# Performance work log

Hardware: AMD Instinct MI355X
Metric: run time of the kernel (lower is better)

Reference implementation:

```python
import jax, jax.numpy as jnp
import numpy as np

HIDDEN = 1024
HEADS = 16
HEAD_DIM = HIDDEN // HEADS
SCALE = HEAD_DIM ** -0.5


def setup_inputs() -> dict:
    key = jax.random.key(0)
    kx, kw, ko = jax.random.split(key, 3)
    x = jax.random.normal(kx, (2, 2048, HIDDEN), dtype=jnp.float32)
    # nn.Linear(hidden, 3*hidden, bias=False): weight shape [3*hidden, hidden]
    w_qkv = jax.random.normal(kw, (3 * HIDDEN, HIDDEN), dtype=jnp.float32) * (HIDDEN ** -0.5)
    w_out = jax.random.normal(ko, (HIDDEN, HIDDEN), dtype=jnp.float32) * (HIDDEN ** -0.5)
    return {"x": x, "w_qkv": w_qkv, "w_out": w_out}


def reference(x, w_qkv, w_out):
    b, s, d = x.shape
    qkv = jnp.einsum('bsd,ed->bse', x, w_qkv)  # [b,s,3d]
    q, k, v = jnp.split(qkv, 3, axis=-1)
    def heads(t):
        return t.reshape(b, s, HEADS, HEAD_DIM).transpose(0, 2, 1, 3)  # [b,h,s,hd]
    q, k, v = heads(q), heads(k), heads(v)
    scores = jnp.einsum('bhqd,bhkd->bhqk', q, k) * SCALE
    attn = jax.nn.softmax(scores, axis=-1)
    out = jnp.einsum('bhqk,bhkd->bhqd', attn, v)
    out = out.transpose(0, 2, 1, 3).reshape(b, s, d)
    return jnp.einsum('bsd,ed->bse', out, w_out)
```

## Files before the change

### kernel.cpp

```cpp
#include <hip/hip_runtime.h>
#include <hip/hip_bf16.h>
#include <stdint.h>

typedef __bf16 bf16;
typedef __bf16 bf16x8 __attribute__((ext_vector_type(8)));
typedef float f32x4 __attribute__((ext_vector_type(4)));
typedef float f32x16 __attribute__((ext_vector_type(16)));

#define HIDDEN 1024
#define HEADS  16
#define HD     64
#define SEQ    2048
#define BATCH  2
#define NTOK   (BATCH*SEQ)
#define E3     (3*HIDDEN)

static __device__ __forceinline__ uint32_t pkbf(float a, float b) {
  union { bf16 h[2]; uint32_t u; } x;
  x.h[0] = (bf16)a; x.h[1] = (bf16)b;
  return x.u;
}

__global__ __launch_bounds__(256) void k_convert(
    const float* __restrict__ x, const float* __restrict__ wqkv, const float* __restrict__ wout,
    bf16* __restrict__ xb, bf16* __restrict__ wqkvb, bf16* __restrict__ woutb)
{
  const int NX = NTOK*HIDDEN/4, NW = E3*HIDDEN/4;
  int i = blockIdx.x*256 + threadIdx.x;
  const float4* s; bf16* d; int o;
  if (i < NX)            { s=(const float4*)x;    d=xb;    o=i; }
  else if (i < NX+NW)    { s=(const float4*)wqkv; d=wqkvb; o=i-NX; }
  else                   { s=(const float4*)wout; d=woutb; o=i-NX-NW; }
  float4 v = s[o];
  union { bf16 b[4]; uint2 u; } p;
  p.b[0]=(bf16)v.x; p.b[1]=(bf16)v.y; p.b[2]=(bf16)v.z; p.b[3]=(bf16)v.w;
  *(uint2*)(d + (size_t)o*4) = p.u;
}

template<int EPI>
__global__ __launch_bounds__(256) void k_gemm(
    const bf16* __restrict__ A, const bf16* __restrict__ B,
    bf16* __restrict__ Oq, bf16* __restrict__ Ok, bf16* __restrict__ Ov,
    float* __restrict__ Of, int M, int N, int K, int nbn)
{
  __shared__ bf16 As[128*32];
  __shared__ bf16 Bs[128*32];
  const int t = threadIdx.x;
  const int lane = t & 63;
  const int w = t >> 6;
  const int g = lane >> 4;
  const int l15 = lane & 15;
  const int wm = (w >> 1) * 64, wn = (w & 1) * 64;
  const int bm = blockIdx.x / nbn, bn = blockIdx.x % nbn;
  const int brow = bm*128, bcol = bn*128;

  f32x4 acc[4][4];
  #pragma unroll
  for (int mi=0;mi<4;mi++)
    #pragma unroll
    for (int ni=0;ni<4;ni++)
      #pragma unroll
      for (int r=0;r<4;r++) acc[mi][ni][r] = 0.f;

  const int nk = K >> 5;
  for (int kt = 0; kt < nk; ++kt) {
    {
      int ch = w*128 + lane;
      const bf16* ga = A + (size_t)(brow + (ch>>2))*K + kt*32 + (ch&3)*8;
      __builtin_amdgcn_global_load_lds((const uint32_t*)ga, (uint32_t*)(As + (w*128)*8), 16, 0, 0);
      const bf16* gb = B + (size_t)(bcol + (ch>>2))*K + kt*32 + (ch&3)*8;
      __builtin_amdgcn_global_load_lds((const uint32_t*)gb, (uint32_t*)(Bs + (w*128)*8), 16, 0, 0);
      ch += 64;
      ga = A + (size_t)(brow + (ch>>2))*K + kt*32 + (ch&3)*8;
      __builtin_amdgcn_global_load_lds((const uint32_t*)ga, (uint32_t*)(As + (w*128+64)*8), 16, 0, 0);
      gb = B + (size_t)(bcol + (ch>>2))*K + kt*32 + (ch&3)*8;
      __builtin_amdgcn_global_load_lds((const uint32_t*)gb, (uint32_t*)(Bs + (w*128+64)*8), 16, 0, 0);
    }
    __syncthreads();
    bf16x8 af[4], bfr[4];
    #pragma unroll
    for (int mi=0;mi<4;mi++) af[mi]  = *(const bf16x8*)(As + (wm + mi*16 + l15)*32 + g*8);
    #pragma unroll
    for (int ni=0;ni<4;ni++) bfr[ni] = *(const bf16x8*)(Bs + (wn + ni*16 + l15)*32 + g*8);
    #pragma unroll
    for (int mi=0;mi<4;mi++)
      #pragma unroll
      for (int ni=0;ni<4;ni++)
        acc[mi][ni] = __builtin_amdgcn_mfma_f32_16x16x32_bf16(af[mi], bfr[ni], acc[mi][ni], 0, 0, 0);
    __syncthreads();
  }

  #pragma unroll
  for (int mi=0;mi<4;mi++) {
    #pragma unroll
    for (int ni=0;ni<4;ni++) {
      #pragma unroll
      for (int r=0;r<4;r++) {
        float val = acc[mi][ni][r];
        int m = brow + wm + mi*16 + 4*g + r;
        int e = bcol + wn + ni*16 + l15;
        if (EPI == 0) {
          int part = e >> 10, we = e & 1023;
          int hh = we >> 6, dd = we & 63;
          int b = m >> 11, sb = m & 2047;
          size_t idx = (((size_t)b*HEADS + hh)*SEQ + sb)*HD + dd;
          if (part == 0)      Oq[idx] = (bf16)(val * 0.125f);
          else if (part == 1) Ok[idx] = (bf16)val;
          else                Ov[idx] = (bf16)val;
        } else {
          Of[(size_t)m*HIDDEN + e] = val;
        }
      }
    }
  }
}

__global__ __launch_bounds__(256) void k_attn(
    const bf16* __restrict__ Qg, const bf16* __restrict__ Kg, const bf16* __restrict__ Vg,
    bf16* __restrict__ Og)
{
  __shared__ bf16 Kl[64*64];
  __shared__ bf16 Vt[64*64];
  const int t = threadIdx.x;
  const int lane = t & 63;
  const int w = t >> 6;
  const int h = lane >> 5;
  const int q = lane & 31;
  const int bh = blockIdx.x >> 4;
  const int qb = blockIdx.x & 15;
  const int q0 = qb*128 + w*32;
  const size_t bhS = (size_t)bh * SEQ * HD;

  bf16x8 qf[4];
  const bf16* qrow = Qg + bhS + (size_t)(q0 + q)*HD;
  #pragma unroll
  for (int s=0;s<4;s++) qf[s] = *(const bf16x8*)(qrow + 16*s + 8*h);

  f32x16 ot[2];
  #pragma unroll
  for (int mf=0;mf<2;mf++)
    #pragma unroll
    for (int r=0;r<16;r++) ot[mf][r]=0.f;
  float mrun = -3.0e38f, lrun = 0.f;

  for (int it=0; it<SEQ/64; ++it) {
    __syncthreads();
    {
      int ch = w*128 + lane;
      int row = ch>>3, o16 = ch&7;
      const bf16* gp = Kg + bhS + (size_t)(it*64+row)*HD + ((o16*8) ^ ((row&7)*8));
      __builtin_amdgcn_global_load_lds((const uint32_t*)gp, (uint32_t*)(Kl + (w*128)*8), 16, 0, 0);
      ch += 64; row = ch>>3; o16 = ch&7;
      gp = Kg + bhS + (size_t)(it*64+row)*HD + ((o16*8) ^ ((row&7)*8));
      __builtin_amdgcn_global_load_lds((const uint32_t*)gp, (uint32_t*)(Kl + (w*128+64)*8), 16, 0, 0);
    }
    {
      int kv0 = (t & 31)*2, d0 = (t>>5)*8;
      const bf16* vg = Vg + bhS + (size_t)(it*64 + kv0)*HD + d0;
      uint4 va = *(const uint4*)vg;
      uint4 vb = *(const uint4*)(vg + HD);
      const uint32_t* pa = (const uint32_t*)&va;
      const uint32_t* pb = (const uint32_t*)&vb;
      #pragma unroll
      for (int jj=0;jj<8;jj++) {
        int dd = d0 + jj;
        uint32_t lo = (jj&1) ? (pa[jj>>1] >> 16) : (pa[jj>>1] & 0xffffu);
        uint32_t hi = (jj&1) ? (pb[jj>>1] >> 16) : (pb[jj>>1] & 0xffffu);
        int byte = (dd*128 + kv0*2) ^ ((dd&7)<<4);
        *(uint32_t*)((char*)Vt + byte) = lo | (hi<<16);
      }
    }
    __syncthreads();

    f32x16 sf[2];
    #pragma unroll
    for (int mf=0;mf<2;mf++)
      #pragma unroll
      for (int r=0;r<16;r++) sf[mf][r]=0.f;
    #pragma unroll
    for (int s=0;s<4;s++) {
      #pragma unroll
      for (int mf=0;mf<2;mf++) {
        int row = mf*32 + q;
        int byte = (row*128 + 32*s + 16*h) ^ ((row&7)<<4);
        bf16x8 kf = *(const bf16x8*)((const char*)Kl + byte);
        sf[mf] = __builtin_amdgcn_mfma_f32_32x32x16_bf16(kf, qf[s], sf[mf], 0,0,0);
      }
    }

    float pm = -3.0e38f;
    #pragma unroll
    for (int mf=0;mf<2;mf++)
      #pragma unroll
      for (int r=0;r<16;r++) pm = fmaxf(pm, sf[mf][r]);
    pm = fmaxf(pm, __shfl_xor(pm, 32, 64));
    float mnew = fmaxf(mrun, pm);
    float alpha = __expf(mrun - mnew);
    float rs = 0.f;
    #pragma unroll
    for (int mf=0;mf<2;mf++)
      #pragma unroll
      for (int r=0;r<16;r++) { float p = __expf(sf[mf][r]-mnew); sf[mf][r]=p; rs += p; }
    rs += __shfl_xor(rs, 32, 64);
    lrun = lrun*alpha + rs;
    mrun = mnew;
    #pragma unroll
    for (int mf=0;mf<2;mf++)
      #pragma unroll
      for (int r=0;r<16;r++) ot[mf][r] *= alpha;

    #pragma unroll
    for (int s=0;s<4;s++) {
      const int f = s>>1, bb = 8*(s&1);
      uint32_t g0A = pkbf(sf[f][bb+0], sf[f][bb+1]);
      uint32_t g0B = pkbf(sf[f][bb+2], sf[f][bb+3]);
      uint32_t g1A = pkbf(sf[f][bb+4], sf[f][bb+5]);
      uint32_t g1B = pkbf(sf[f][bb+6], sf[f][bb+7]);
      uint32_t ownA = h ? g1A : g0A, ownB = h ? g1B : g0B;
      uint32_t sndA = h ? g0A : g1A, sndB = h ? g0B : g1B;
      uint32_t rcvA = __shfl_xor(sndA, 32, 64);
      uint32_t rcvB = __shfl_xor(sndB, 32, 64);
      union { uint32_t u[4]; bf16x8 v; } pf;
      if (h == 0) { pf.u[0]=ownA; pf.u[1]=ownB; pf.u[2]=rcvA; pf.u[3]=rcvB; }
      else        { pf.u[0]=rcvA; pf.u[1]=rcvB; pf.u[2]=ownA; pf.u[3]=ownB; }
      #pragma unroll
      for (int mf=0;mf<2;mf++) {
        int row = mf*32 + q;
        int byte = (row*128 + 32*s + 16*h) ^ ((row&7)<<4);
        bf16x8 vf = *(const bf16x8*)((const char*)Vt + byte);
        ot[mf] = __builtin_amdgcn_mfma_f32_32x32x16_bf16(vf, pf.v, ot[mf], 0,0,0);
      }
    }
  }

  float inv = 1.0f / lrun;
  int b = bh >> 4, head = bh & 15;
  size_t orow = ((size_t)b*SEQ + q0 + q)*HIDDEN + head*HD;
  #pragma unroll
  for (int mf=0;mf<2;mf++)
    #pragma unroll
    for (int r=0;r<16;r++) {
      int dd = mf*32 + (r&3) + 8*(r>>2) + 4*h;
      Og[orow + dd] = (bf16)(ot[mf][r]*inv);
    }
}

extern "C" void kernel_launch(void* const* d_in, const int* in_sizes, int n_in,
                              void* d_out, int out_size, void* d_ws, size_t ws_size,
                              hipStream_t stream)
{
  (void)in_sizes; (void)n_in; (void)out_size; (void)ws_size;
  const float* x    = (const float*)d_in[0];
  const float* wqkv = (const float*)d_in[1];
  const float* wout = (const float*)d_in[2];
  float* out = (float*)d_out;
  char* ws = (char*)d_ws;
  bf16* xb    = (bf16*)(ws);
  bf16* wqkvb = (bf16*)(ws + 8388608);
  bf16* woutb = (bf16*)(ws + 14680064);
  bf16* Q     = (bf16*)(ws + 16777216);
  bf16* K     = (bf16*)(ws + 25165824);
  bf16* V     = (bf16*)(ws + 33554432);
  bf16* O     = (bf16*)(ws + 41943040);

  k_convert<<<8192, 256, 0, stream>>>(x, wqkv, wout, xb, wqkvb, woutb);
  k_gemm<0><<<32*24, 256, 0, stream>>>(xb, wqkvb, Q, K, V, nullptr, NTOK, E3, HIDDEN, 24);
  k_attn<<<512, 256, 0, stream>>>(Q, K, V, O);
  k_gemm<1><<<32*8, 256, 0, stream>>>(O, woutb, nullptr, nullptr, nullptr, out, NTOK, HIDDEN, HIDDEN, 8);
}
```

Before: 214.0 us.

## Double-buffer attention K/V tiles, use exp2 with lazy rescale, shrink out-proj tile

Attention now double-buffers the K and V shared-memory tiles, prefetching the next block while computing the current one, and drops one barrier per iteration. Softmax folds log2(e) into the Q scale so it can use exp2. It only rescales the running max and accumulator when the new max exceeds the old one by more than 8, which removes most rescale multiplies. The output-projection GEMM uses a 64-row tile so it launches 512 blocks instead of 256, improving occupancy on the small GEMM. The costs are double the attention LDS footprint and a possible precision risk from the lazy rescale threshold.

After: 229.7 us. 7.3% more time.

```diff
diff --git a/kernel.cpp b/kernel.cpp
--- a/kernel.cpp
+++ b/kernel.cpp
@@ -14,6 +14,8 @@
 #define BATCH  2
 #define NTOK   (BATCH*SEQ)
 #define E3     (3*HIDDEN)
+
+#define QSCALE (0.125f * 1.44269504088896f)
 
 static __device__ __forceinline__ uint32_t pkbf(float a, float b) {
   union { bf16 h[2]; uint32_t u; } x;
@@ -37,26 +39,27 @@
   *(uint2*)(d + (size_t)o*4) = p.u;
 }
 
-template<int EPI>
+template<int EPI, int BM>
 __global__ __launch_bounds__(256) void k_gemm(
     const bf16* __restrict__ A, const bf16* __restrict__ B,
     bf16* __restrict__ Oq, bf16* __restrict__ Ok, bf16* __restrict__ Ov,
     float* __restrict__ Of, int M, int N, int K, int nbn)
 {
-  __shared__ bf16 As[128*32];
+  constexpr int MI = BM/32;
+  __shared__ bf16 As[BM*32];
   __shared__ bf16 Bs[128*32];
   const int t = threadIdx.x;
   const int lane = t & 63;
   const int w = t >> 6;
   const int g = lane >> 4;
   const int l15 = lane & 15;
-  const int wm = (w >> 1) * 64, wn = (w & 1) * 64;
+  const int wm = (w >> 1) * (BM/2), wn = (w & 1) * 64;
   const int bm = blockIdx.x / nbn, bn = blockIdx.x % nbn;
-  const int brow = bm*128, bcol = bn*128;
-
-  f32x4 acc[4][4];
-  #pragma unroll
-  for (int mi=0;mi<4;mi++)
+  const int brow = bm*BM, bcol = bn*128;
+
+  f32x4 acc[MI][4];
+  #pragma unroll
+  for (int mi=0;mi<MI;mi++)
     #pragma unroll
     for (int ni=0;ni<4;ni++)
       #pragma unroll
@@ -64,26 +67,34 @@
 
   const int nk = K >> 5;
   for (int kt = 0; kt < nk; ++kt) {
-    {
+    if constexpr (BM == 128) {
       int ch = w*128 + lane;
       const bf16* ga = A + (size_t)(brow + (ch>>2))*K + kt*32 + (ch&3)*8;
       __builtin_amdgcn_global_load_lds((const uint32_t*)ga, (uint32_t*)(As + (w*128)*8), 16, 0, 0);
+      int ch2 = ch + 64;
+      const bf16* ga2 = A + (size_t)(brow + (ch2>>2))*K + kt*32 + (ch2&3)*8;
+      __builtin_amdgcn_global_load_lds((const uint32_t*)ga2, (uint32_t*)(As + (w*128+64)*8), 16, 0, 0);
+    } else {
+      int ch = w*64 + lane;
+      const bf16* ga = A + (size_t)(brow + (ch>>2))*K + kt*32 + (ch&3)*8;
+      __builtin_amdgcn_global_load_lds((const uint32_t*)ga, (uint32_t*)(As + (w*64)*8), 16, 0, 0);
+    }
+    {
+      int ch = w*128 + lane;
       const bf16* gb = B + (size_t)(bcol + (ch>>2))*K + kt*32 + (ch&3)*8;
       __builtin_amdgcn_global_load_lds((const uint32_t*)gb, (uint32_t*)(Bs + (w*128)*8), 16, 0, 0);
-      ch += 64;
-      ga = A + (size_t)(brow + (ch>>2))*K + kt*32 + (ch&3)*8;
-      __builtin_amdgcn_global_load_lds((const uint32_t*)ga, (uint32_t*)(As + (w*128+64)*8), 16, 0, 0);
-      gb = B + (size_t)(bcol + (ch>>2))*K + kt*32 + (ch&3)*8;
-      __builtin_amdgcn_global_load_lds((const uint32_t*)gb, (uint32_t*)(Bs + (w*128+64)*8), 16, 0, 0);
+      int ch2 = ch + 64;
+      const bf16* gb2 = B + (size_t)(bcol + (ch2>>2))*K + kt*32 + (ch2&3)*8;
+      __builtin_amdgcn_global_load_lds((const uint32_t*)gb2, (uint32_t*)(Bs + (w*128+64)*8), 16, 0, 0);
     }
     __syncthreads();
-    bf16x8 af[4], bfr[4];
-    #pragma unroll
-    for (int mi=0;mi<4;mi++) af[mi]  = *(const bf16x8*)(As + (wm + mi*16 + l15)*32 + g*8);
+    bf16x8 af[MI], bfr[4];
+    #pragma unroll
+    for (int mi=0;mi<MI;mi++) af[mi]  = *(const bf16x8*)(As + (wm + mi*16 + l15)*32 + g*8);
     #pragma unroll
     for (int ni=0;ni<4;ni++) bfr[ni] = *(const bf16x8*)(Bs + (wn + ni*16 + l15)*32 + g*8);
     #pragma unroll
-    for (int mi=0;mi<4;mi++)
+    for (int mi=0;mi<MI;mi++)
       #pragma unroll
       for (int ni=0;ni<4;ni++)
         acc[mi][ni] = __builtin_amdgcn_mfma_f32_16x16x32_bf16(af[mi], bfr[ni], acc[mi][ni], 0, 0, 0);
@@ -91,7 +102,7 @@
   }
 
   #pragma unroll
-  for (int mi=0;mi<4;mi++) {
+  for (int mi=0;mi<MI;mi++) {
     #pragma unroll
     for (int ni=0;ni<4;ni++) {
       #pragma unroll
@@ -104,7 +115,7 @@
           int hh = we >> 6, dd = we & 63;
           int b = m >> 11, sb = m & 2047;
           size_t idx = (((size_t)b*HEADS + hh)*SEQ + sb)*HD + dd;
-          if (part == 0)      Oq[idx] = (bf16)(val * 0.125f);
+          if (part == 0)      Oq[idx] = (bf16)(val * QSCALE);
           else if (part == 1) Ok[idx] = (bf16)val;
           else                Ov[idx] = (bf16)val;
         } else {
@@ -119,8 +130,8 @@
     const bf16* __restrict__ Qg, const bf16* __restrict__ Kg, const bf16* __restrict__ Vg,
     bf16* __restrict__ Og)
 {
-  __shared__ bf16 Kl[64*64];
-  __shared__ bf16 Vt[64*64];
+  __shared__ bf16 Kl[2][64*64];
+  __shared__ bf16 Vt[2][64*64];
   const int t = threadIdx.x;
   const int lane = t & 63;
   const int w = t >> 6;
@@ -143,34 +154,50 @@
     for (int r=0;r<16;r++) ot[mf][r]=0.f;
   float mrun = -3.0e38f, lrun = 0.f;
 
-  for (int it=0; it<SEQ/64; ++it) {
-    __syncthreads();
-    {
-      int ch = w*128 + lane;
-      int row = ch>>3, o16 = ch&7;
-      const bf16* gp = Kg + bhS + (size_t)(it*64+row)*HD + ((o16*8) ^ ((row&7)*8));
-      __builtin_amdgcn_global_load_lds((const uint32_t*)gp, (uint32_t*)(Kl + (w*128)*8), 16, 0, 0);
-      ch += 64; row = ch>>3; o16 = ch&7;
-      gp = Kg + bhS + (size_t)(it*64+row)*HD + ((o16*8) ^ ((row&7)*8));
-      __builtin_amdgcn_global_load_lds((const uint32_t*)gp, (uint32_t*)(Kl + (w*128+64)*8), 16, 0, 0);
-    }
-    {
-      int kv0 = (t & 31)*2, d0 = (t>>5)*8;
-      const bf16* vg = Vg + bhS + (size_t)(it*64 + kv0)*HD + d0;
-      uint4 va = *(const uint4*)vg;
-      uint4 vb = *(const uint4*)(vg + HD);
-      const uint32_t* pa = (const uint32_t*)&va;
-      const uint32_t* pb = (const uint32_t*)&vb;
-      #pragma unroll
-      for (int jj=0;jj<8;jj++) {
-        int dd = d0 + jj;
-        uint32_t lo = (jj&1) ? (pa[jj>>1] >> 16) : (pa[jj>>1] & 0xffffu);
-        uint32_t hi = (jj&1) ? (pb[jj>>1] >> 16) : (pb[jj>>1] & 0xffffu);
-        int byte = (dd*128 + kv0*2) ^ ((dd&7)<<4);
-        *(uint32_t*)((char*)Vt + byte) = lo | (hi<<16);
-      }
-    }
-    __syncthreads();
+  const int kvv0 = (t & 31)*2, dd0 = (t>>5)*8;
+
+  auto stageK = [&](int it, int buf) {
+    int ch = w*128 + lane;
+    int row = ch>>3, o16 = ch&7;
+    const bf16* gp = Kg + bhS + (size_t)(it*64+row)*HD + ((o16*8) ^ ((row&7)*8));
+    __builtin_amdgcn_global_load_lds((const uint32_t*)gp, (uint32_t*)(&Kl[buf][0] + (size_t)(w*128)*8), 16, 0, 0);
+    int ch2 = ch + 64;
+    int row2 = ch2>>3, o16b = ch2&7;
+    const bf16* gp2 = Kg + bhS + (size_t)(it*64+row2)*HD + ((o16b*8) ^ ((row2&7)*8));
+    __builtin_amdgcn_global_load_lds((const uint32_t*)gp2, (uint32_t*)(&Kl[buf][0] + (size_t)(w*128+64)*8), 16, 0, 0);
+  };
+  auto loadV = [&](int it, uint4& va, uint4& vb) {
+    const bf16* vg = Vg + bhS + (size_t)(it*64 + kvv0)*HD + dd0;
+    va = *(const uint4*)vg;
+    vb = *(const uint4*)(vg + HD);
+  };
+  auto writeVt = [&](uint4 va, uint4 vb, int buf) {
+    const uint32_t* pa = (const uint32_t*)&va;
+    const uint32_t* pb = (const uint32_t*)&vb;
+    #pragma unroll
+    for (int jj=0;jj<8;jj++) {
+      int dd = dd0 + jj;
+      uint32_t lo = (jj&1) ? (pa[jj>>1] >> 16) : (pa[jj>>1] & 0xffffu);
+      uint32_t hi = (jj&1) ? (pb[jj>>1] >> 16) : (pb[jj>>1] & 0xffffu);
+      int byte = (dd*128 + kvv0*2) ^ ((dd&7)<<4);
+      *(uint32_t*)((char*)&Vt[buf][0] + byte) = lo | (hi<<16);
+    }
+  };
+
+  {
+    uint4 va, vb;
+    stageK(0, 0);
+    loadV(0, va, vb);
+    writeVt(va, vb, 0);
+  }
+  __syncthreads();
+
+  const int NT = SEQ/64;
+  for (int it=0; it<NT; ++it) {
+    const int cur = it & 1;
+    const bool pre = (it+1) < NT;
+    uint4 na, nb;
+    if (pre) { stageK(it+1, cur^1); loadV(it+1, na, nb); }
 
     f32x16 sf[2];
     #pragma unroll
@@ -183,31 +210,37 @@
       for (int mf=0;mf<2;mf++) {
         int row = mf*32 + q;
         int byte = (row*128 + 32*s + 16*h) ^ ((row&7)<<4);
-        bf16x8 kf = *(const bf16x8*)((const char*)Kl + byte);
+        bf16x8 kf = *(const bf16x8*)((const char*)&Kl[cur][0] + byte);
         sf[mf] = __builtin_amdgcn_mfma_f32_32x32x16_bf16(kf, qf[s], sf[mf], 0,0,0);
       }
     }
 
-    float pm = -3.0e38f;
+    float mx[16];
+    #pragma unroll
+    for (int r=0;r<16;r++) mx[r] = fmaxf(sf[0][r], sf[1][r]);
+    #pragma unroll
+    for (int dstep=8; dstep; dstep>>=1)
+      #pragma unroll
+      for (int r=0;r<8;r++) if (r < dstep) mx[r] = fmaxf(mx[r], mx[r+dstep]);
+    float pm = fmaxf(mx[0], __shfl_xor(mx[0], 32, 64));
+
+    if (__any(pm - mrun > 8.f)) {
+      float mnew = fmaxf(mrun, pm);
+      float alpha = exp2f(mrun - mnew);
+      lrun *= alpha;
+      #pragma unroll
+      for (int mf=0;mf<2;mf++)
+        #pragma unroll
+        for (int r=0;r<16;r++) ot[mf][r] *= alpha;
+      mrun = mnew;
+    }
+    float rs = 0.f;
     #pragma unroll
     for (int mf=0;mf<2;mf++)
       #pragma unroll
-      for (int r=0;r<16;r++) pm = fmaxf(pm, sf[mf][r]);
-    pm = fmaxf(pm, __shfl_xor(pm, 32, 64));
-    float mnew = fmaxf(mrun, pm);
-    float alpha = __expf(mrun - mnew);
-    float rs = 0.f;
-    #pragma unroll
-    for (int mf=0;mf<2;mf++)
-      #pragma unroll
-      for (int r=0;r<16;r++) { float p = __expf(sf[mf][r]-mnew); sf[mf][r]=p; rs += p; }
+      for (int r=0;r<16;r++) { float p = exp2f(sf[mf][r]-mrun); sf[mf][r]=p; rs += p; }
     rs += __shfl_xor(rs, 32, 64);
-    lrun = lrun*alpha + rs;
-    mrun = mnew;
-    #pragma unroll
-    for (int mf=0;mf<2;mf++)
-      #pragma unroll
-      for (int r=0;r<16;r++) ot[mf][r] *= alpha;
+    lrun += rs;
 
     #pragma unroll
     for (int s=0;s<4;s++) {
@@ -227,10 +260,13 @@
       for (int mf=0;mf<2;mf++) {
         int row = mf*32 + q;
         int byte = (row*128 + 32*s + 16*h) ^ ((row&7)<<4);
-        bf16x8 vf = *(const bf16x8*)((const char*)Vt + byte);
+        bf16x8 vf = *(const bf16x8*)((const char*)&Vt[cur][0] + byte);
         ot[mf] = __builtin_amdgcn_mfma_f32_32x32x16_bf16(vf, pf.v, ot[mf], 0,0,0);
       }
     }
+
+    if (pre) writeVt(na, nb, cur^1);
+    __syncthreads();
   }
 
   float inv = 1.0f / lrun;
@@ -264,7 +300,7 @@
   bf16* O     = (bf16*)(ws + 41943040);
 
   k_convert<<<8192, 256, 0, stream>>>(x, wqkv, wout, xb, wqkvb, woutb);
-  k_gemm<0><<<32*24, 256, 0, stream>>>(xb, wqkvb, Q, K, V, nullptr, NTOK, E3, HIDDEN, 24);
+  k_gemm<0,128><<<32*24, 256, 0, stream>>>(xb, wqkvb, Q, K, V, nullptr, NTOK, E3, HIDDEN, 24);
   k_attn<<<512, 256, 0, stream>>>(Q, K, V, O);
-  k_gemm<1><<<32*8, 256, 0, stream>>>(O, woutb, nullptr, nullptr, nullptr, out, NTOK, HIDDEN, HIDDEN, 8);
-}
+  k_gemm<1,64><<<64*8, 256, 0, stream>>>(O, woutb, nullptr, nullptr, nullptr, out, NTOK, HIDDEN, HIDDEN, 8);
+}
```
